# Performance work log

Measured on AMD Instinct MI355X. Metric: run time of the kernel, lower is better.

## Reference

```python
import jax, jax.numpy as jnp
import numpy as np

B, S, E = 2, 2048, 2048
HQ, HKV, D = 16, 4, 128
WINDOW = 512
ROPE_BASE = 10000.0


def apply_rope(x):
    # x: [B, H, S, D]; rotate-half RoPE, positions start at 0 (prefill, no cache)
    half = x.shape[-1] // 2
    inv_freq = 1.0 / (ROPE_BASE ** (jnp.arange(half, dtype=jnp.float32) / half))
    ang = jnp.arange(x.shape[2], dtype=jnp.float32)[:, None] * inv_freq[None, :]  # [S, half]
    cos, sin = jnp.cos(ang), jnp.sin(ang)
    x1, x2 = x[..., :half], x[..., half:]
    return jnp.concatenate([x1 * cos - x2 * sin, x1 * sin + x2 * cos], axis=-1)


def setup_inputs() -> dict:
    key = jax.random.key(0)
    ks = jax.random.split(key, 9)
    sc = 0.02
    return {
        "x": jax.random.normal(ks[0], (B, S, E), dtype=jnp.float32),
        "Wq": jax.random.normal(ks[1], (HQ * D, E), dtype=jnp.float32) * sc,
        "bq": jnp.zeros((HQ * D,), dtype=jnp.float32),
        "Wk": jax.random.normal(ks[2], (HKV * D, E), dtype=jnp.float32) * sc,
        "bk": jnp.zeros((HKV * D,), dtype=jnp.float32),
        "Wv": jax.random.normal(ks[3], (HKV * D, E), dtype=jnp.float32) * sc,
        "bv": jnp.zeros((HKV * D,), dtype=jnp.float32),
        "Wo": jax.random.normal(ks[4], (E, HQ * D), dtype=jnp.float32) * sc,
        "bo": jnp.zeros((E,), dtype=jnp.float32),
    }


def reference(x, Wq, bq, Wk, bk, Wv, bv, Wo, bo):
    b, s, _ = x.shape
    group = HQ // HKV
    # projections (torch Linear: y = x @ W.T + b)
    Q = (x @ Wq.T + bq).reshape(b, s, HQ, D).transpose(0, 2, 1, 3)     # [B,HQ,S,D]
    K = (x @ Wk.T + bk).reshape(b, s, HKV, D).transpose(0, 2, 1, 3)    # [B,HKV,S,D]
    V = (x @ Wv.T + bv).reshape(b, s, HKV, D).transpose(0, 2, 1, 3)
    Q = apply_rope(Q)
    K = apply_rope(K)
    # GQA: group query heads per KV head instead of repeating K/V (same math)
    Qg = Q.reshape(b, HKV, group, s, D)
    scores = jnp.einsum('bkgqd,bkyd->bkgqy', Qg, K) / jnp.sqrt(jnp.float32(D))
    # sliding-window causal mask: j <= i and i - j <= window_size
    i = jnp.arange(s)[:, None]
    j = jnp.arange(s)[None, :]
    allowed = (j <= i) & ((i - j) <= WINDOW)
    scores = jnp.where(allowed, scores, jnp.float32(-jnp.inf))
    w = jax.nn.softmax(scores, axis=-1)
    out = jnp.einsum('bkgqy,bkyd->bkgqd', w, V)                        # [B,HKV,G,S,D]
    out = out.reshape(b, HQ, s, D).transpose(0, 2, 1, 3).reshape(b, s, HQ * D)
    out = out @ Wo.T + bo  # dropout is identity at inference
    return out
```

## Files before the change

kernel.cpp:

```cpp
#include <hip/hip_runtime.h>
#include <hip/hip_bf16.h>

typedef unsigned short u16;
typedef unsigned int u32;
typedef __attribute__((ext_vector_type(4))) unsigned short ushort4_t;
typedef __attribute__((ext_vector_type(8))) short short8;
typedef __attribute__((ext_vector_type(4))) float f32x4;

#define B_ 2
#define S_ 2048
#define E_ 2048
#define HQ_ 16
#define HKV_ 4
#define D_ 128
#define WINDOW_ 512

static __device__ __forceinline__ float bf2f(u16 u) {
    union { unsigned int i; float f; } v; v.i = ((unsigned int)u) << 16; return v.f;
}
static __device__ __forceinline__ u16 f2bf(float f) {
    unsigned int x = __float_as_uint(f);
    unsigned int r = (x + 0x7fffu + ((x >> 16) & 1u)) >> 16;
    return (u16)r;
}

static __device__ __forceinline__ void gload_lds16(const u16* g, u16* l) {
    __builtin_amdgcn_global_load_lds(
        (const __attribute__((address_space(1))) unsigned int*)g,
        (__attribute__((address_space(3))) unsigned int*)l,
        16, 0, 0);
}

static __device__ __forceinline__ int detect_fp32(const u16* wq, int* cnt_sh) {
    if (threadIdx.x == 0) *cnt_sh = 0;
    __syncthreads();
    int c = 0;
    #pragma unroll
    for (int k = 0; k < 4; ++k) {
        u16 v = wq[threadIdx.x * 4 + k];
        if (((v >> 7) & 0xFF) >= 0x90) c++;
    }
    atomicAdd(cnt_sh, c);
    __syncthreads();
    return (*cnt_sh >= 64) ? 1 : 0;
}

#define C_WQ   8388608u
#define C_WK   12582912u
#define C_WV   13631488u
#define C_BQ   14680064u
#define C_BK   14682112u
#define C_BV   14682624u
#define C_WO   14683136u
#define C_BO   18877440u
#define NTOT   18879488u

__global__ __launch_bounds__(256) void convert_kernel(
    const void* p0, const void* p1, const void* p2, const void* p3, const void* p4,
    const void* p5, const void* p6, const void* p7, const void* p8,
    u16* __restrict__ C, int* __restrict__ flagout)
{
    __shared__ int cnt;
    const int f = detect_fp32((const u16*)p1, &cnt);
    if (blockIdx.x == 0 && threadIdx.x == 0) *flagout = f;

    unsigned int idx = (blockIdx.x * 256u + threadIdx.x) * 4u;
    if (idx >= NTOT) return;

    const void* src; unsigned int local;
    if      (idx < C_WQ) { src = p0; local = idx; }
    else if (idx < C_WK) { src = p1; local = idx - C_WQ; }
    else if (idx < C_WV) { src = p3; local = idx - C_WK; }
    else if (idx < C_BQ) { src = p5; local = idx - C_WV; }
    else if (idx < C_BK) { src = p2; local = idx - C_BQ; }
    else if (idx < C_BV) { src = p4; local = idx - C_BK; }
    else if (idx < C_WO) { src = p6; local = idx - C_BV; }
    else if (idx < C_BO) { src = p7; local = idx - C_WO; }
    else                 { src = p8; local = idx - C_BO; }

    ushort4_t o;
    if (f) {
        float4 v = *(const float4*)((const float*)src + local);
        o[0] = f2bf(v.x); o[1] = f2bf(v.y); o[2] = f2bf(v.z); o[3] = f2bf(v.w);
    } else {
        o = *(const ushort4_t*)((const u16*)src + local);
    }
    *(ushort4_t*)(C + idx) = o;
}

__global__ __launch_bounds__(512, 2) void gemm256(
    const u16* __restrict__ A, const u16* __restrict__ W,
    const u16* __restrict__ bias, u16* __restrict__ C,
    int M, int N, int K)
{
    __shared__ __align__(16) u16 lds[65536];

    const int m0 = blockIdx.y * 256, n0 = blockIdx.x * 256;
    const int t = threadIdx.x;
    const int wv = t >> 6, lane = t & 63;
    const int wm = wv >> 2, wn = wv & 3;
    const int quad = lane >> 4, l16 = lane & 15;
    const int h3 = l16 & 7;

    const int rr = t >> 3;
    const int sblk = ((t & 7) ^ (rr & 7)) * 8;

    const u16* Asrc = A + (size_t)(m0 + rr) * K + sblk;
    const u16* Bsrc = W + (size_t)(n0 + rr) * K + sblk;
    u16* ldsA = lds + wv * 512;
    u16* ldsB = lds + 16384 + wv * 512;

#define STAGE_A(slot, Qi, k0) gload_lds16(Asrc + (size_t)((Qi) * 64) * K + (k0), ldsA + (slot) * 32768 + (Qi) * 4096)
#define STAGE_B(slot, Qi, k0) gload_lds16(Bsrc + (size_t)((Qi) * 64) * K + (k0), ldsB + (slot) * 32768 + (Qi) * 4096)

    f32x4 acc[8][4];
    #pragma unroll
    for (int mi = 0; mi < 8; ++mi)
        #pragma unroll
        for (int ni = 0; ni < 4; ++ni)
            acc[mi][ni] = (f32x4){0.f, 0.f, 0.f, 0.f};

    const int NT = K / 64;

    #pragma unroll
    for (int q = 0; q < 4; ++q) STAGE_A(0, q, 0);
    #pragma unroll
    for (int q = 0; q < 4; ++q) STAGE_B(0, q, 0);
    __builtin_amdgcn_sched_barrier(0);
    STAGE_A(1, 0, 64);
    STAGE_A(1, 2, 64);
    __builtin_amdgcn_sched_barrier(0);

    short8 aA[4][2], aB[4][2];
    short8 b0[2][2], b1[2][2];

#define DSREAD_A(dst, qm_)                                                     \
    _Pragma("unroll")                                                          \
    for (int fr = 0; fr < 4; ++fr) {                                           \
        const int r = wm * 128 + (qm_) * 64 + fr * 16 + l16;                   \
        _Pragma("unroll")                                                      \
        for (int kk = 0; kk < 2; ++kk)                                         \
            dst[fr][kk] = *(const short8*)(As + r * 64 + (((kk * 4 + quad) ^ h3) << 3)); \
    }

#define DSREAD_B(dst, qn_)                                                     \
    _Pragma("unroll")                                                          \
    for (int g = 0; g < 2; ++g) {                                              \
        const int r = wn * 64 + (qn_) * 32 + g * 16 + l16;                     \
        _Pragma("unroll")                                                      \
        for (int kk = 0; kk < 2; ++kk)                                         \
            dst[g][kk] = *(const short8*)(Bs + r * 64 + (((kk * 4 + quad) ^ h3) << 3)); \
    }

#define MFMA_PH(qm_, afrag, bfrag, qn_)                                        \
    __builtin_amdgcn_s_setprio(1);                                             \
    _Pragma("unroll")                                                          \
    for (int g = 0; g < 2; ++g)                                                \
        _Pragma("unroll")                                                      \
        for (int fr = 0; fr < 4; ++fr)                                         \
            _Pragma("unroll")                                                  \
            for (int kk = 0; kk < 2; ++kk)                                     \
                acc[(qm_) * 4 + fr][(qn_) * 2 + g] =                           \
                    __builtin_amdgcn_mfma_f32_16x16x32_bf16(                   \
                        afrag[fr][kk], bfrag[g][kk], acc[(qm_) * 4 + fr][(qn_) * 2 + g], 0, 0, 0); \
    __builtin_amdgcn_s_setprio(0);

    for (int kt = 0; kt < NT; ++kt) {
        const int slot = kt & 1;
        const u16* As = lds + slot * 32768;
        const u16* Bs = As + 16384;

        if (kt == NT - 1) asm volatile("s_waitcnt vmcnt(0)" ::: "memory");
        else              asm volatile("s_waitcnt vmcnt(2)" ::: "memory");
        __builtin_amdgcn_s_barrier();
        __builtin_amdgcn_sched_barrier(0);

        const int kB = (kt + 1) * 64;
        const int kA = (kt + 2) * 64;
        const int sB = slot ^ 1;
        const bool doEarly = (kt <= NT - 2);
        const bool doMid   = (kt <= NT - 3);

        DSREAD_A(aA, 0);
        DSREAD_B(b0, 0);
        __builtin_amdgcn_sched_barrier(0);
        DSREAD_B(b1, 1);
        __builtin_amdgcn_sched_barrier(0);

        if (doEarly) { STAGE_A(sB, 1, kB); STAGE_A(sB, 3, kB);
                       STAGE_B(sB, 0, kB); STAGE_B(sB, 1, kB);
                       STAGE_B(sB, 2, kB); STAGE_B(sB, 3, kB); }
        __builtin_amdgcn_sched_barrier(0);

        asm volatile("s_waitcnt lgkmcnt(4)" ::: "memory");
        __builtin_amdgcn_sched_barrier(0);
        DSREAD_A(aB, 1);
        __builtin_amdgcn_sched_barrier(0);

        MFMA_PH(0, aA, b0, 0);
        __builtin_amdgcn_sched_barrier(0);
        asm volatile("s_waitcnt lgkmcnt(8)" ::: "memory");
        __builtin_amdgcn_sched_barrier(0);
        MFMA_PH(0, aA, b1, 1);
        __builtin_amdgcn_sched_barrier(0);
        asm volatile("s_waitcnt lgkmcnt(0)" ::: "memory");
        __builtin_amdgcn_sched_barrier(0);
        __builtin_amdgcn_s_barrier();
        __builtin_amdgcn_sched_barrier(0);

        if (doMid) { STAGE_A(slot, 0, kA); STAGE_A(slot, 2, kA); }
        __builtin_amdgcn_sched_barrier(0);

        MFMA_PH(1, aB, b1, 1);
        __builtin_amdgcn_sched_barrier(0);
        MFMA_PH(1, aB, b0, 0);
        __builtin_amdgcn_sched_barrier(0);
    }

#undef STAGE_A
#undef STAGE_B
#undef DSREAD_A
#undef DSREAD_B
#undef MFMA_PH

    #pragma unroll
    for (int mi = 0; mi < 8; ++mi) {
        #pragma unroll
        for (int ni = 0; ni < 4; ++ni) {
            const int row0 = m0 + wm * 128 + mi * 16 + quad * 4;
            const int col  = n0 + wn * 64 + ni * 16 + l16;
            const float bb = bf2f(bias[col]);
            #pragma unroll
            for (int r = 0; r < 4; ++r)
                C[(size_t)(row0 + r) * N + col] = f2bf(acc[mi][ni][r] + bb);
        }
    }
}

#define TBK 32

__global__ __launch_bounds__(256) void gemm128_out(
    const u16* __restrict__ A, const u16* __restrict__ W,
    const u16* __restrict__ bias, void* __restrict__ Cout,
    int M, int N, int K, const int* __restrict__ flagp)
{
    __shared__ __align__(16) u16 As[128 * TBK];
    __shared__ __align__(16) u16 Bs[128 * TBK];

    const int m0 = blockIdx.y * 128, n0 = blockIdx.x * 128;

    const int t = threadIdx.x;
    const int wv = t >> 6, lane = t & 63;
    const int waveM = wv >> 1, waveN = wv & 1;
    const int quad = lane >> 4, l16 = lane & 15;

    const int lrow = lane >> 2;
    const int lcol = (lane & 3) * 8;

    f32x4 acc[4][4];
    #pragma unroll
    for (int mi = 0; mi < 4; ++mi)
        #pragma unroll
        for (int ni = 0; ni < 4; ++ni)
            acc[mi][ni] = (f32x4){0.f, 0.f, 0.f, 0.f};

    const u16* ga = A + (size_t)(m0 + wv * 32 + lrow) * K + lcol;
    const u16* gb = W + (size_t)(n0 + wv * 32 + lrow) * K + lcol;
    u16* la0 = As + (wv * 32) * TBK;
    u16* la1 = As + (wv * 32 + 16) * TBK;
    u16* lb0 = Bs + (wv * 32) * TBK;
    u16* lb1 = Bs + (wv * 32 + 16) * TBK;

    for (int k0 = 0; k0 < K; k0 += TBK) {
        __syncthreads();
        gload_lds16(ga + k0, la0);
        gload_lds16(ga + k0 + (size_t)16 * K, la1);
        gload_lds16(gb + k0, lb0);
        gload_lds16(gb + k0 + (size_t)16 * K, lb1);
        __syncthreads();

        short8 af[4];
        #pragma unroll
        for (int mi = 0; mi < 4; ++mi)
            af[mi] = *(const short8*)(As + (waveM * 64 + mi * 16 + l16) * TBK + quad * 8);
        #pragma unroll
        for (int ni = 0; ni < 4; ++ni) {
            short8 bf = *(const short8*)(Bs + (waveN * 64 + ni * 16 + l16) * TBK + quad * 8);
            #pragma unroll
            for (int mi = 0; mi < 4; ++mi)
                acc[mi][ni] = __builtin_amdgcn_mfma_f32_16x16x32_bf16(af[mi], bf, acc[mi][ni], 0, 0, 0);
        }
    }

    const int f = *flagp;
    #pragma unroll
    for (int mi = 0; mi < 4; ++mi) {
        #pragma unroll
        for (int ni = 0; ni < 4; ++ni) {
            int row0 = m0 + waveM * 64 + mi * 16 + quad * 4;
            int col  = n0 + waveN * 64 + ni * 16 + l16;
            float bb = bf2f(bias[col]);
            #pragma unroll
            for (int r = 0; r < 4; ++r) {
                float val = acc[mi][ni][r] + bb;
                size_t idx = (size_t)(row0 + r) * N + col;
                if (f) ((float*)Cout)[idx] = val;
                else   ((u16*)Cout)[idx]   = f2bf(val);
            }
        }
    }
}

#define ROPE_BLOCKS 20480

__global__ __launch_bounds__(256) void rope_transpose(
    u16* __restrict__ QKV, u16* __restrict__ VT)
{
    if (blockIdx.x < ROPE_BLOCKS) {
        const size_t qtot = (size_t)B_ * S_ * HQ_ * 64;
        size_t idx = (size_t)blockIdx.x * 256 + threadIdx.x;

        int d; size_t tok; u16* p;
        if (idx < qtot) {
            d = (int)(idx & 63);
            size_t th = idx >> 6;
            int h = (int)(th & 15);
            tok = th >> 4;
            p = QKV + tok * 3072 + h * 128 + d;
        } else {
            size_t r = idx - qtot;
            d = (int)(r & 63);
            size_t th = r >> 6;
            int kh = (int)(th & 3);
            tok = th >> 2;
            p = QKV + tok * 3072 + 2048 + kh * 128 + d;
        }
        int s = (int)(tok & (S_ - 1));

        float x1 = bf2f(p[0]);
        float x2 = bf2f(p[64]);
        float inv_freq = __expf(-0.14391156514f * (float)d);
        float ang = (float)s * inv_freq;
        float sn, cs;
        __sincosf(ang, &sn, &cs);
        p[0]  = f2bf(x1 * cs - x2 * sn);
        p[64] = f2bf(x1 * sn + x2 * cs);
    } else {
        const int bid = blockIdx.x - ROPE_BLOCKS;
        const int t = threadIdx.x;
        const int s_blk = bid & 63;
        const int dh = (bid >> 6) & 1;
        const int bkh = bid >> 7;
        const int b = bkh >> 2, kh = bkh & 3;

        const int d = dh * 64 + (t & 63);
        const int s0 = s_blk * 32 + (t >> 6) * 8;

        const u16* src = QKV + (size_t)(b * S_ + s0) * 3072 + 2560 + kh * 128 + d;
        short8 v;
        #pragma unroll
        for (int j = 0; j < 8; ++j)
            v[j] = (short)src[(size_t)j * 3072];
        *(short8*)(VT + ((size_t)(bkh * 128 + d)) * S_ + s0) = v;
    }
}

__global__ __launch_bounds__(256) void attn_mfma(
    const u16* __restrict__ QKV, const u16* __restrict__ VT, u16* __restrict__ O)
{
    __shared__ __align__(16) u16 Ks[32 * 136];
    __shared__ __align__(16) u16 Vs[128 * 40];
    __shared__ __align__(16) u16 ps[4][16 * 40];

    const int t = threadIdx.x;
    const int wv = t >> 6, lane = t & 63;
    const int quad = lane >> 4, l16 = lane & 15;

    const int h = blockIdx.x & 15;
    const int tile = (blockIdx.x >> 4) & 31;
    const int b = blockIdx.x >> 9;
    const int kh = h >> 2;

    const int i0b = tile * 64;
    const int i0w = i0b + wv * 16;
    const float scale = 0.08838834764831845f;
    const float CEXP = 8.0f;

    short8 qf[4];
    {
        const u16* qrow = QKV + (size_t)(b * S_ + i0w + l16) * 3072 + h * 128 + quad * 8;
        #pragma unroll
        for (int kc = 0; kc < 4; ++kc)
            qf[kc] = *(const short8*)(qrow + kc * 32);
    }

    short8 ones;
    #pragma unroll
    for (int j = 0; j < 8; ++j) ones[j] = (short)0x3F80;

    f32x4 oc[8];
    #pragma unroll
    for (int c = 0; c < 8; ++c) oc[c] = (f32x4){0.f, 0.f, 0.f, 0.f};
    f32x4 ocl = (f32x4){0.f, 0.f, 0.f, 0.f};

    int jlo = i0b - WINDOW_; if (jlo < 0) jlo = 0;
    const int nblk = (i0b + 64 - jlo) >> 5;

    const u16* VTb = VT + (size_t)(b * 4 + kh) * 128 * S_;

    for (int blk = 0; blk < nblk; ++blk) {
        const int jbase = jlo + blk * 32;
        __syncthreads();
        #pragma unroll
        for (int it = 0; it < 2; ++it) {
            int idx = it * 256 + t;
            int key = idx >> 4;
            int c8  = (idx & 15) * 8;
            int row = ((key & 1) << 4) | (key >> 1);
            short8 kvv = *(const short8*)(QKV + (size_t)(b * S_ + jbase + key) * 3072 + 2048 + kh * 128 + c8);
            *(short8*)(Ks + row * 136 + c8) = kvv;
        }
        #pragma unroll
        for (int it = 0; it < 2; ++it) {
            int idx = it * 256 + t;
            int d = idx >> 2;
            int q4 = idx & 3;
            short8 vvv = *(const short8*)(VTb + (size_t)d * S_ + jbase + q4 * 8);
            *(short8*)(Vs + d * 40 + q4 * 8) = vvv;
        }
        __syncthreads();

        bool active = (jbase <= i0w + 15) && (jbase + 31 >= i0w - WINDOW_);
        if (!active) continue;

        f32x4 sc0 = {0.f,0.f,0.f,0.f}, sc1 = {0.f,0.f,0.f,0.f};
        #pragma unroll
        for (int kc = 0; kc < 4; ++kc) {
            short8 kb0 = *(const short8*)(Ks + l16 * 136 + kc * 32 + quad * 8);
            short8 kb1 = *(const short8*)(Ks + (16 + l16) * 136 + kc * 32 + quad * 8);
            sc0 = __builtin_amdgcn_mfma_f32_16x16x32_bf16(qf[kc], kb0, sc0, 0, 0, 0);
            sc1 = __builtin_amdgcn_mfma_f32_16x16x32_bf16(qf[kc], kb1, sc1, 0, 0, 0);
        }

        const int j0 = jbase + 2 * l16;
        const int iq = i0w + quad * 4;
        u16* pw = ps[wv];
        #pragma unroll
        for (int r = 0; r < 4; ++r) {
            int i = iq + r;
            bool ok0 = (unsigned)(i - j0)     <= (unsigned)WINDOW_;
            bool ok1 = (unsigned)(i - j0 - 1) <= (unsigned)WINDOW_;
            float p0 = ok0 ? __expf(sc0[r] * scale - CEXP) : 0.f;
            float p1 = ok1 ? __expf(sc1[r] * scale - CEXP) : 0.f;
            u32 pk = ((u32)f2bf(p1) << 16) | (u32)f2bf(p0);
            *(u32*)(pw + (quad * 4 + r) * 40 + 2 * l16) = pk;
        }
        short8 pa = *(const short8*)(pw + l16 * 40 + quad * 8);

        #pragma unroll
        for (int c = 0; c < 8; ++c) {
            short8 vb = *(const short8*)(Vs + (c * 16 + l16) * 40 + quad * 8);
            oc[c] = __builtin_amdgcn_mfma_f32_16x16x32_bf16(pa, vb, oc[c], 0, 0, 0);
        }
        ocl = __builtin_amdgcn_mfma_f32_16x16x32_bf16(pa, ones, ocl, 0, 0, 0);
    }

    float inv0[4];
    #pragma unroll
    for (int r = 0; r < 4; ++r) inv0[r] = 1.0f / ocl[r];
    #pragma unroll
    for (int c = 0; c < 8; ++c) {
        #pragma unroll
        for (int r = 0; r < 4; ++r) {
            O[((size_t)(b * S_ + i0w + quad * 4 + r) * HQ_ + h) * D_ + c * 16 + l16] =
                f2bf(oc[c][r] * inv0[r]);
        }
    }
}

extern "C" void kernel_launch(void* const* d_in, const int* in_sizes, int n_in,
                              void* d_out, int out_size, void* d_ws, size_t ws_size,
                              hipStream_t stream)
{
    char* ws = (char*)d_ws;
    u16* Cc   = (u16*)ws;
    int* flag = (int*)(ws + 37758976);
    u16* QKV  = (u16*)(ws + 37759232);
    u16* Ab   = (u16*)(ws + 37759232 + 25165824);

    const u16* xb    = Cc;
    u16*       VT    = Cc;
    const u16* Wqkv  = Cc + C_WQ;
    const u16* bqkv  = Cc + C_BQ;
    const u16* Wob   = Cc + C_WO;
    const u16* bob   = Cc + C_BO;

    const int M = B_ * S_;
    dim3 blk(256);

    convert_kernel<<<dim3(NTOT / 4 / 256), blk, 0, stream>>>(
        d_in[0], d_in[1], d_in[2], d_in[3], d_in[4], d_in[5], d_in[6], d_in[7], d_in[8],
        Cc, flag);

    gemm256<<<dim3(3072 / 256, M / 256), dim3(512), 0, stream>>>(
        xb, Wqkv, bqkv, QKV, M, 3072, E_);

    rope_transpose<<<dim3(ROPE_BLOCKS + 1024), blk, 0, stream>>>(QKV, VT);

    attn_mfma<<<dim3(B_ * HQ_ * (S_ / 64)), blk, 0, stream>>>(QKV, VT, Ab);

    gemm128_out<<<dim3(E_ / 128, M / 128), blk, 0, stream>>>(Ab, Wob, bob, d_out, M, E_, HQ_ * D_, flag);
}
```

Before: 313.6 us.

## Rewrite output projection GEMM with double-buffered swizzled LDS pipeline

Replaces the simple 128x128 output-projection GEMM with a 128x256-tile, 512-thread kernel that double-buffers K=64 tiles in LDS. It uses XOR-swizzled LDS layout, explicit waitcnt/barrier scheduling and priority hints so async global-to-LDS loads overlap MFMA work. The aim is to hide memory latency and cut the per-iteration double sync of the old kernel. It adds far more LDS per block, which lowers occupancy, and the hand-tuned wait counts are easy to get wrong.

```diff
diff --git a/kernel.cpp b/kernel.cpp
--- a/kernel.cpp
+++ b/kernel.cpp
@@ -237,25 +237,30 @@
     }
 }
 
-#define TBK 32
-
-__global__ __launch_bounds__(256) void gemm128_out(
+__global__ __launch_bounds__(512, 2) void gemm_out_p(
     const u16* __restrict__ A, const u16* __restrict__ W,
     const u16* __restrict__ bias, void* __restrict__ Cout,
     int M, int N, int K, const int* __restrict__ flagp)
 {
-    __shared__ __align__(16) u16 As[128 * TBK];
-    __shared__ __align__(16) u16 Bs[128 * TBK];
-
-    const int m0 = blockIdx.y * 128, n0 = blockIdx.x * 128;
-
+    __shared__ __align__(16) u16 lds[49152];
+
+    const int m0 = blockIdx.y * 128, n0 = blockIdx.x * 256;
     const int t = threadIdx.x;
     const int wv = t >> 6, lane = t & 63;
-    const int waveM = wv >> 1, waveN = wv & 1;
+    const int wm = wv >> 2, wn = wv & 3;
     const int quad = lane >> 4, l16 = lane & 15;
-
-    const int lrow = lane >> 2;
-    const int lcol = (lane & 3) * 8;
+    const int h3 = l16 & 7;
+
+    const int rr = t >> 3;
+    const int sblk = ((t & 7) ^ (rr & 7)) * 8;
+
+    const u16* Asrc = A + (size_t)(m0 + rr) * K + sblk;
+    const u16* Bsrc = W + (size_t)(n0 + rr) * K + sblk;
+    u16* ldsA = lds + wv * 512;
+    u16* ldsB = lds + 8192 + wv * 512;
+
+#define STAGE_A(slot, Qi, k0) gload_lds16(Asrc + (size_t)((Qi) * 64) * K + (k0), ldsA + (slot) * 24576 + (Qi) * 4096)
+#define STAGE_B(slot, Qi, k0) gload_lds16(Bsrc + (size_t)((Qi) * 64) * K + (k0), ldsB + (slot) * 24576 + (Qi) * 4096)
 
     f32x4 acc[4][4];
     #pragma unroll
@@ -264,42 +269,106 @@
         for (int ni = 0; ni < 4; ++ni)
             acc[mi][ni] = (f32x4){0.f, 0.f, 0.f, 0.f};
 
-    const u16* ga = A + (size_t)(m0 + wv * 32 + lrow) * K + lcol;
-    const u16* gb = W + (size_t)(n0 + wv * 32 + lrow) * K + lcol;
-    u16* la0 = As + (wv * 32) * TBK;
-    u16* la1 = As + (wv * 32 + 16) * TBK;
-    u16* lb0 = Bs + (wv * 32) * TBK;
-    u16* lb1 = Bs + (wv * 32 + 16) * TBK;
-
-    for (int k0 = 0; k0 < K; k0 += TBK) {
-        __syncthreads();
-        gload_lds16(ga + k0, la0);
-        gload_lds16(ga + k0 + (size_t)16 * K, la1);
-        gload_lds16(gb + k0, lb0);
-        gload_lds16(gb + k0 + (size_t)16 * K, lb1);
-        __syncthreads();
-
-        short8 af[4];
-        #pragma unroll
-        for (int mi = 0; mi < 4; ++mi)
-            af[mi] = *(const short8*)(As + (waveM * 64 + mi * 16 + l16) * TBK + quad * 8);
+    const int NT = K / 64;
+
+    STAGE_A(0, 0, 0); STAGE_A(0, 1, 0);
+    STAGE_B(0, 0, 0); STAGE_B(0, 1, 0); STAGE_B(0, 2, 0); STAGE_B(0, 3, 0);
+    __builtin_amdgcn_sched_barrier(0);
+    STAGE_A(1, 0, 64);
+    __builtin_amdgcn_sched_barrier(0);
+
+    short8 aA[4][2];
+    short8 b0[2][2], b1[2][2];
+
+#define DSREAD_A(dst)                                                          \
+    _Pragma("unroll")                                                          \
+    for (int fr = 0; fr < 4; ++fr) {                                           \
+        const int r = wm * 64 + fr * 16 + l16;                                 \
+        _Pragma("unroll")                                                      \
+        for (int kk = 0; kk < 2; ++kk)                                         \
+            dst[fr][kk] = *(const short8*)(As + r * 64 + (((kk * 4 + quad) ^ h3) << 3)); \
+    }
+
+#define DSREAD_B(dst, qn_)                                                     \
+    _Pragma("unroll")                                                          \
+    for (int g = 0; g < 2; ++g) {                                              \
+        const int r = wn * 64 + (qn_) * 32 + g * 16 + l16;                     \
+        _Pragma("unroll")                                                      \
+        for (int kk = 0; kk < 2; ++kk)                                         \
+            dst[g][kk] = *(const short8*)(Bs + r * 64 + (((kk * 4 + quad) ^ h3) << 3)); \
+    }
+
+#define MFMA_PH(bfrag, qn_)                                                    \
+    __builtin_amdgcn_s_setprio(1);                                             \
+    _Pragma("unroll")                                                          \
+    for (int g = 0; g < 2; ++g)                                                \
+        _Pragma("unroll")                                                      \
+        for (int fr = 0; fr < 4; ++fr)                                         \
+            _Pragma("unroll")                                                  \
+            for (int kk = 0; kk < 2; ++kk)                                     \
+                acc[fr][(qn_) * 2 + g] =                                       \
+                    __builtin_amdgcn_mfma_f32_16x16x32_bf16(                   \
+                        aA[fr][kk], bfrag[g][kk], acc[fr][(qn_) * 2 + g], 0, 0, 0); \
+    __builtin_amdgcn_s_setprio(0);
+
+    for (int kt = 0; kt < NT; ++kt) {
+        const int slot = kt & 1;
+        const u16* As = lds + slot * 24576;
+        const u16* Bs = As + 8192;
+
+        if (kt == NT - 1) asm volatile("s_waitcnt vmcnt(0)" ::: "memory");
+        else              asm volatile("s_waitcnt vmcnt(1)" ::: "memory");
+        __builtin_amdgcn_s_barrier();
+        __builtin_amdgcn_sched_barrier(0);
+
+        const int kB = (kt + 1) * 64;
+        const int kA = (kt + 2) * 64;
+        const int sB = slot ^ 1;
+        const bool doEarly = (kt <= NT - 2);
+        const bool doMid   = (kt <= NT - 3);
+
+        DSREAD_A(aA);
+        DSREAD_B(b0, 0);
+        __builtin_amdgcn_sched_barrier(0);
+        DSREAD_B(b1, 1);
+        __builtin_amdgcn_sched_barrier(0);
+
+        if (doEarly) { STAGE_A(sB, 1, kB);
+                       STAGE_B(sB, 0, kB); STAGE_B(sB, 1, kB);
+                       STAGE_B(sB, 2, kB); STAGE_B(sB, 3, kB); }
+        __builtin_amdgcn_sched_barrier(0);
+
+        asm volatile("s_waitcnt lgkmcnt(4)" ::: "memory");
+        __builtin_amdgcn_sched_barrier(0);
+
+        MFMA_PH(b0, 0);
+        __builtin_amdgcn_sched_barrier(0);
+        asm volatile("s_waitcnt lgkmcnt(0)" ::: "memory");
+        __builtin_amdgcn_sched_barrier(0);
+        __builtin_amdgcn_s_barrier();
+        __builtin_amdgcn_sched_barrier(0);
+
+        if (doMid) { STAGE_A(slot, 0, kA); }
+        __builtin_amdgcn_sched_barrier(0);
+
+        MFMA_PH(b1, 1);
+        __builtin_amdgcn_sched_barrier(0);
+    }
+
+#undef STAGE_A
+#undef STAGE_B
+#undef DSREAD_A
+#undef DSREAD_B
+#undef MFMA_PH
+
+    const int f = *flagp;
+    #pragma unroll
+    for (int mi = 0; mi < 4; ++mi) {
         #pragma unroll
         for (int ni = 0; ni < 4; ++ni) {
-            short8 bf = *(const short8*)(Bs + (waveN * 64 + ni * 16 + l16) * TBK + quad * 8);
-            #pragma unroll
-            for (int mi = 0; mi < 4; ++mi)
-                acc[mi][ni] = __builtin_amdgcn_mfma_f32_16x16x32_bf16(af[mi], bf, acc[mi][ni], 0, 0, 0);
-        }
-    }
-
-    const int f = *flagp;
-    #pragma unroll
-    for (int mi = 0; mi < 4; ++mi) {
-        #pragma unroll
-        for (int ni = 0; ni < 4; ++ni) {
-            int row0 = m0 + waveM * 64 + mi * 16 + quad * 4;
-            int col  = n0 + waveN * 64 + ni * 16 + l16;
-            float bb = bf2f(bias[col]);
+            const int row0 = m0 + wm * 64 + mi * 16 + quad * 4;
+            const int col  = n0 + wn * 64 + ni * 16 + l16;
+            const float bb = bf2f(bias[col]);
             #pragma unroll
             for (int r = 0; r < 4; ++r) {
                 float val = acc[mi][ni][r] + bb;
@@ -509,5 +578,6 @@
 
     attn_mfma<<<dim3(B_ * HQ_ * (S_ / 64)), blk, 0, stream>>>(QKV, VT, Ab);
 
-    gemm128_out<<<dim3(E_ / 128, M / 128), blk, 0, stream>>>(Ab, Wob, bob, d_out, M, E_, HQ_ * D_, flag);
-}
+    gemm_out_p<<<dim3(E_ / 256, M / 128), dim3(512), 0, stream>>>(
+        Ab, Wob, bob, d_out, M, E_, HQ_ * D_, flag);
+}
```

Measured after the change: 295.4 us. 1.06x faster.
